# Performance work log

Measured on AMD Instinct MI355X. Metric: run time of the kernel, lower is better.

## Reference

```python
import jax, jax.numpy as jnp
import numpy as np

N_NODES = 50000
N_EDGES = 800000
IN_CH = 256
OUT_CH = 128
HID = 2 * OUT_CH  # 256
N_GRAPHS = 64


def setup_inputs() -> dict:
    key = jax.random.key(0)
    k = jax.random.split(key, 8)
    x = jax.random.normal(k[0], (N_NODES, IN_CH), dtype=jnp.float32)
    edge_index = jax.random.randint(k[1], (2, N_EDGES), 0, N_NODES, dtype=jnp.int64)
    batch = jnp.sort(jax.random.randint(k[2], (N_NODES,), 0, N_GRAPHS, dtype=jnp.int64))
    # GCNConv parameters (glorot-ish init)
    W1 = jax.random.normal(k[3], (IN_CH, HID), dtype=jnp.float32) / np.sqrt(IN_CH)
    b1 = jnp.zeros((HID,), dtype=jnp.float32)
    W2 = jax.random.normal(k[4], (HID, OUT_CH), dtype=jnp.float32) / np.sqrt(HID)
    b2 = jnp.zeros((OUT_CH,), dtype=jnp.float32)
    return {"x": x, "W1": W1, "b1": b1, "W2": W2, "b2": b2,
            "edge_index": edge_index, "batch": batch}


def _gcn_conv(x, W, b, src, dst, n):
    """PyG GCNConv: transform, then sym-normalized aggregation with self-loops."""
    h = x @ W  # [N, F_out]
    # degree over destination nodes, including the added self-loop
    deg = jnp.zeros((n,), dtype=h.dtype).at[dst].add(1.0) + 1.0
    dinv = jax.lax.rsqrt(deg)
    norm = dinv[src] * dinv[dst]            # [E]
    agg = jnp.zeros_like(h).at[dst].add(h[src] * norm[:, None])
    agg = agg + h * (1.0 / deg)[:, None]    # self-loop contribution: deg_i^{-1}
    return agg + b


def reference(x, W1, b1, W2, b2, edge_index, batch):
    src, dst = edge_index[0], edge_index[1]
    # dropout is identity in eval mode (training=False)
    h = jax.nn.elu(_gcn_conv(x, W1, b1, src, dst, N_NODES))
    h = _gcn_conv(h, W2, b2, src, dst, N_NODES)
    # global mean pool over graphs
    ones = jnp.ones((N_NODES,), dtype=h.dtype)
    counts = jax.ops.segment_sum(ones, batch, num_segments=N_GRAPHS)
    sums = jax.ops.segment_sum(h, batch, num_segments=N_GRAPHS)
    return sums / jnp.maximum(counts, 1.0)[:, None]
```

## Files before the change

### kernel.cpp

```cpp
#include <hip/hip_runtime.h>
#include <hip/hip_bf16.h>

#define N_NODES 50000
#define N_EDGES 800000
#define IN_CH 256
#define HID 256
#define OUT_CH 128
#define N_GRAPHS 64
#define SCAN_BLOCKS 196
#define M_PAD 50048
#define POOL_CHUNK 32
#define POOL_BLOCKS ((N_NODES + POOL_CHUNK - 1) / POOL_CHUNK)

typedef __bf16 bf16x8 __attribute__((ext_vector_type(8)));
typedef float f32x4 __attribute__((ext_vector_type(4)));

__device__ __forceinline__ float bf2f(unsigned short u) {
    union { unsigned int i; float f; } x; x.i = ((unsigned int)u) << 16; return x.f;
}
__device__ __forceinline__ unsigned short f2bf(float f) {
    union { float f; unsigned int i; } x; x.f = f;
    unsigned int r = x.i + 0x7FFFu + ((x.i >> 16) & 1u);
    return (unsigned short)(r >> 16);
}

__device__ __forceinline__ void load16(const void* g, void* l) {
    __builtin_amdgcn_global_load_lds(
        (const __attribute__((address_space(1))) void*)g,
        (__attribute__((address_space(3))) void*)l, 16, 0, 0);
}

__global__ __launch_bounds__(256) void count_kernel(const int* __restrict__ ei,
                                                    int* __restrict__ cnt) {
    int e = blockIdx.x * 256 + threadIdx.x;
    if (e < N_EDGES) atomicAdd(&cnt[ei[N_EDGES + e]], 1);
}

__global__ __launch_bounds__(256) void scan_a_kernel(const int* __restrict__ cnt,
                                                     int* __restrict__ rowptr,
                                                     int* __restrict__ blocksum,
                                                     float* __restrict__ dinv,
                                                     float* __restrict__ invdeg) {
    __shared__ int tmp[256];
    int t = threadIdx.x;
    int i = blockIdx.x * 256 + t;
    int v = (i < N_NODES) ? cnt[i] : 0;
    int x = v;
    tmp[t] = x;
    __syncthreads();
#pragma unroll
    for (int off = 1; off < 256; off <<= 1) {
        int y = (t >= off) ? tmp[t - off] : 0;
        __syncthreads();
        x += y;
        tmp[t] = x;
        __syncthreads();
    }
    if (i < N_NODES) {
        rowptr[i] = x - v;
        float d = (float)v + 1.0f;
        dinv[i] = rsqrtf(d);
        invdeg[i] = 1.0f / d;
    }
    if (t == 255) blocksum[blockIdx.x] = x;
}

__global__ __launch_bounds__(256) void scan_b_kernel(const int* __restrict__ blocksum,
                                                     int* __restrict__ blockoff,
                                                     int* __restrict__ rowptr) {
    __shared__ int tmp[256];
    int t = threadIdx.x;
    int v = (t < SCAN_BLOCKS) ? blocksum[t] : 0;
    int x = v;
    tmp[t] = x;
    __syncthreads();
#pragma unroll
    for (int off = 1; off < 256; off <<= 1) {
        int y = (t >= off) ? tmp[t - off] : 0;
        __syncthreads();
        x += y;
        tmp[t] = x;
        __syncthreads();
    }
    if (t < SCAN_BLOCKS) blockoff[t] = x - v;
    if (t == 255) rowptr[N_NODES] = x;
}

__global__ __launch_bounds__(256) void scan_c_kernel(int* __restrict__ rowptr,
                                                     const int* __restrict__ blockoff) {
    int i = blockIdx.x * 256 + threadIdx.x;
    if (i < N_NODES) rowptr[i] += blockoff[blockIdx.x];
}

__global__ __launch_bounds__(256) void fill_kernel(const int* __restrict__ ei,
                                                   const int* __restrict__ rowptr,
                                                   int* __restrict__ fillp,
                                                   int2* __restrict__ edge2,
                                                   const float* __restrict__ dinv) {
    int e = blockIdx.x * 256 + threadIdx.x;
    if (e >= N_EDGES) return;
    int s = ei[e];
    int d = ei[N_EDGES + e];
    int p = rowptr[d] + atomicAdd(&fillp[d], 1);
    float w = dinv[s] * dinv[d];
    edge2[p] = make_int2(s, __float_as_int(w));
}

__global__ __launch_bounds__(256) void cvt_x_kernel(const float* __restrict__ x,
                                                    unsigned short* __restrict__ xb) {
    int i = blockIdx.x * 256 + threadIdx.x;
    if (i >= M_PAD * (IN_CH / 4)) return;
    ushort4 o;
    if (i < N_NODES * (IN_CH / 4)) {
        float4 v = ((const float4*)x)[i];
        o.x = f2bf(v.x); o.y = f2bf(v.y); o.z = f2bf(v.z); o.w = f2bf(v.w);
    } else {
        o = make_ushort4(0, 0, 0, 0);
    }
    ((ushort4*)xb)[i] = o;
}

__global__ __launch_bounds__(256) void cvt_w_kernel(const float* __restrict__ W1,
                                                    const float* __restrict__ W2,
                                                    unsigned short* __restrict__ w1t,
                                                    unsigned short* __restrict__ w2t) {
    int i = blockIdx.x * 256 + threadIdx.x;
    if (i < HID * IN_CH) {
        int n = i >> 8, k = i & 255;
        w1t[i] = f2bf(W1[k * HID + n]);
    } else if (i < HID * IN_CH + OUT_CH * HID) {
        int j = i - HID * IN_CH;
        int n = j >> 8, k = j & 255;
        w2t[j] = f2bf(W2[k * OUT_CH + n]);
    }
}

__global__ __launch_bounds__(256) void gemm_mfma_kernel(
        const unsigned short* __restrict__ A,
        const unsigned short* __restrict__ Bt,
        unsigned short* __restrict__ C,
        int N) {
    const int K = 256;
    __shared__ char As[8192];
    __shared__ char Bs[8192];
    int tid = threadIdx.x;
    int bm = blockIdx.x * 128;
    int bn = blockIdx.y * 128;
    int lane = tid & 63, wave = tid >> 6;
    int lane15 = lane & 15, quad = lane >> 4;
    int wm0 = (wave >> 1) << 6;
    int wn0 = (wave & 1) << 6;

    int s1 = tid, s2 = tid + 256;
    int r1 = s1 >> 2, q1 = (s1 & 3) ^ ((r1 >> 1) & 3);
    int r2 = s2 >> 2, q2 = (s2 & 3) ^ ((r2 >> 1) & 3);
    const char* gA1 = (const char*)(A + (size_t)(bm + r1) * K) + (q1 << 4);
    const char* gA2 = (const char*)(A + (size_t)(bm + r2) * K) + (q2 << 4);
    const char* gB1 = (const char*)(Bt + (size_t)(bn + r1) * K) + (q1 << 4);
    const char* gB2 = (const char*)(Bt + (size_t)(bn + r2) * K) + (q2 << 4);
    char* lA1 = As + (wave << 10);
    char* lA2 = As + 4096 + (wave << 10);
    char* lB1 = Bs + (wave << 10);
    char* lB2 = Bs + 4096 + (wave << 10);

    int swm = (lane15 >> 1) & 3;
    f32x4 acc[4][4];
#pragma unroll
    for (int mt = 0; mt < 4; mt++)
#pragma unroll
        for (int nt = 0; nt < 4; nt++)
            acc[mt][nt] = (f32x4){0.f, 0.f, 0.f, 0.f};

    for (int k0 = 0; k0 < K; k0 += 32) {
        __syncthreads();
        load16(gA1 + (k0 << 1), lA1);
        load16(gA2 + (k0 << 1), lA2);
        load16(gB1 + (k0 << 1), lB1);
        load16(gB2 + (k0 << 1), lB2);
        __syncthreads();
        bf16x8 af[4], bfr[4];
#pragma unroll
        for (int t = 0; t < 4; t++) {
            int ra = wm0 + t * 16 + lane15;
            af[t] = *(const bf16x8*)(As + ra * 64 + ((quad ^ swm) << 4));
            int rb = wn0 + t * 16 + lane15;
            bfr[t] = *(const bf16x8*)(Bs + rb * 64 + ((quad ^ swm) << 4));
        }
#pragma unroll
        for (int mt = 0; mt < 4; mt++)
#pragma unroll
            for (int nt = 0; nt < 4; nt++)
                acc[mt][nt] = __builtin_amdgcn_mfma_f32_16x16x32_bf16(
                    af[mt], bfr[nt], acc[mt][nt], 0, 0, 0);
    }

#pragma unroll
    for (int mt = 0; mt < 4; mt++) {
        int rowb = bm + wm0 + mt * 16 + quad * 4;
#pragma unroll
        for (int nt = 0; nt < 4; nt++) {
            int col = bn + wn0 + nt * 16 + lane15;
            f32x4 a = acc[mt][nt];
            C[(size_t)(rowb + 0) * N + col] = f2bf(a[0]);
            C[(size_t)(rowb + 1) * N + col] = f2bf(a[1]);
            C[(size_t)(rowb + 2) * N + col] = f2bf(a[2]);
            C[(size_t)(rowb + 3) * N + col] = f2bf(a[3]);
        }
    }
}

__global__ __launch_bounds__(256) void agg1_kernel(const unsigned short* __restrict__ h,
                                                   const float* __restrict__ bias,
                                                   const int* __restrict__ rowptr,
                                                   const int2* __restrict__ edge2,
                                                   const float* __restrict__ invdeg,
                                                   unsigned short* __restrict__ out) {
    int node = blockIdx.x * 4 + (threadIdx.x >> 6);
    if (node >= N_NODES) return;
    int lane = threadIdx.x & 63;
    const ushort4* h4 = (const ushort4*)h;
    float id = invdeg[node];
    ushort4 sv = h4[(size_t)node * 64 + lane];
    float4 acc = make_float4(bf2f(sv.x) * id, bf2f(sv.y) * id,
                             bf2f(sv.z) * id, bf2f(sv.w) * id);
    int e0 = rowptr[node], e1 = rowptr[node + 1];
    int e = e0;
    for (; e + 1 < e1; e += 2) {
        int2 ed0 = edge2[e], ed1 = edge2[e + 1];
        float w0 = __int_as_float(ed0.y), w1 = __int_as_float(ed1.y);
        ushort4 v0 = h4[(size_t)ed0.x * 64 + lane];
        ushort4 v1 = h4[(size_t)ed1.x * 64 + lane];
        acc.x += bf2f(v0.x) * w0; acc.y += bf2f(v0.y) * w0;
        acc.z += bf2f(v0.z) * w0; acc.w += bf2f(v0.w) * w0;
        acc.x += bf2f(v1.x) * w1; acc.y += bf2f(v1.y) * w1;
        acc.z += bf2f(v1.z) * w1; acc.w += bf2f(v1.w) * w1;
    }
    if (e < e1) {
        int2 ed0 = edge2[e];
        float w0 = __int_as_float(ed0.y);
        ushort4 v0 = h4[(size_t)ed0.x * 64 + lane];
        acc.x += bf2f(v0.x) * w0; acc.y += bf2f(v0.y) * w0;
        acc.z += bf2f(v0.z) * w0; acc.w += bf2f(v0.w) * w0;
    }
    float4 bb = ((const float4*)bias)[lane];
    acc.x += bb.x; acc.y += bb.y; acc.z += bb.z; acc.w += bb.w;
    acc.x = acc.x > 0.f ? acc.x : expm1f(acc.x);
    acc.y = acc.y > 0.f ? acc.y : expm1f(acc.y);
    acc.z = acc.z > 0.f ? acc.z : expm1f(acc.z);
    acc.w = acc.w > 0.f ? acc.w : expm1f(acc.w);
    ushort4 o;
    o.x = f2bf(acc.x); o.y = f2bf(acc.y); o.z = f2bf(acc.z); o.w = f2bf(acc.w);
    ((ushort4*)out)[(size_t)node * 64 + lane] = o;
}

__global__ __launch_bounds__(256) void agg2_kernel(const unsigned short* __restrict__ h,
                                                   const float* __restrict__ bias,
                                                   const int* __restrict__ rowptr,
                                                   const int2* __restrict__ edge2,
                                                   const float* __restrict__ invdeg,
                                                   float* __restrict__ out) {
    int node = blockIdx.x * 4 + (threadIdx.x >> 6);
    if (node >= N_NODES) return;
    int lane = threadIdx.x & 63;
    const ushort2* h2 = (const ushort2*)h;
    float id = invdeg[node];
    ushort2 sv = h2[(size_t)node * 64 + lane];
    float2 acc = make_float2(bf2f(sv.x) * id, bf2f(sv.y) * id);
    int e0 = rowptr[node], e1 = rowptr[node + 1];
    int e = e0;
    for (; e + 1 < e1; e += 2) {
        int2 ed0 = edge2[e], ed1 = edge2[e + 1];
        float w0 = __int_as_float(ed0.y), w1 = __int_as_float(ed1.y);
        ushort2 v0 = h2[(size_t)ed0.x * 64 + lane];
        ushort2 v1 = h2[(size_t)ed1.x * 64 + lane];
        acc.x += bf2f(v0.x) * w0; acc.y += bf2f(v0.y) * w0;
        acc.x += bf2f(v1.x) * w1; acc.y += bf2f(v1.y) * w1;
    }
    if (e < e1) {
        int2 ed0 = edge2[e];
        float w0 = __int_as_float(ed0.y);
        ushort2 v0 = h2[(size_t)ed0.x * 64 + lane];
        acc.x += bf2f(v0.x) * w0; acc.y += bf2f(v0.y) * w0;
    }
    float2 bb = ((const float2*)bias)[lane];
    acc.x += bb.x; acc.y += bb.y;
    ((float2*)out)[(size_t)node * 64 + lane] = acc;
}

__global__ __launch_bounds__(128) void pool_kernel(const float* __restrict__ h,
                                                   const int* __restrict__ batch,
                                                   float* __restrict__ pool,
                                                   float* __restrict__ gcnt) {
    int c = threadIdx.x;
    int n0 = blockIdx.x * POOL_CHUNK;
    int n1 = n0 + POOL_CHUNK;
    if (n1 > N_NODES) n1 = N_NODES;
    if (n0 >= N_NODES) return;
    float run = 0.f, cnt = 0.f;
    int g = batch[n0];
    for (int n = n0; n < n1; n++) {
        int gn = batch[n];
        if (gn != g) {
            atomicAdd(&pool[g * OUT_CH + c], run);
            if (c == 0) atomicAdd(&gcnt[g], cnt);
            run = 0.f; cnt = 0.f; g = gn;
        }
        run += h[(size_t)n * OUT_CH + c];
        if (c == 0) cnt += 1.f;
    }
    atomicAdd(&pool[g * OUT_CH + c], run);
    if (c == 0) atomicAdd(&gcnt[g], cnt);
}

__global__ __launch_bounds__(256) void final_kernel(const float* __restrict__ pool,
                                                    const float* __restrict__ gcnt,
                                                    float* __restrict__ out) {
    int i = blockIdx.x * 256 + threadIdx.x;
    if (i < N_GRAPHS * OUT_CH)
        out[i] = pool[i] / fmaxf(gcnt[i >> 7], 1.0f);
}

extern "C" void kernel_launch(void* const* d_in, const int* in_sizes, int n_in,
                              void* d_out, int out_size, void* d_ws, size_t ws_size,
                              hipStream_t stream) {
    const float* x  = (const float*)d_in[0];
    const float* W1 = (const float*)d_in[1];
    const float* b1 = (const float*)d_in[2];
    const float* W2 = (const float*)d_in[3];
    const float* b2 = (const float*)d_in[4];
    const int*   ei = (const int*)d_in[5];
    const int*   batch = (const int*)d_in[6];
    float* out = (float*)d_out;

    unsigned short* xb  = (unsigned short*)d_ws;
    unsigned short* h1b = xb  + (size_t)M_PAD * HID;
    unsigned short* hBb = h1b + (size_t)M_PAD * HID;
    unsigned short* h2b = hBb + (size_t)M_PAD * HID;
    unsigned short* w1t = h2b + (size_t)M_PAD * OUT_CH;
    unsigned short* w2t = w1t + HID * IN_CH;
    float* hC  = (float*)xb;
    float* dinv   = (float*)(w2t + OUT_CH * HID);
    float* invdeg = dinv + N_NODES;
    int*   rowptr = (int*)(invdeg + N_NODES);
    int2*  edge2  = (int2*)(rowptr + 50016);
    int*   cnt    = (int*)(edge2 + N_EDGES);
    int*   fillp  = cnt + N_NODES;
    float* gcnt   = (float*)(fillp + N_NODES);
    float* pool   = gcnt + N_GRAPHS;
    int*   blocksum = (int*)(pool + N_GRAPHS * OUT_CH);
    int*   blockoff = blocksum + 256;

    size_t zbytes = ((size_t)N_NODES * 2 + N_GRAPHS + (size_t)N_GRAPHS * OUT_CH) * 4;
    hipMemsetAsync(cnt, 0, zbytes, stream);

    count_kernel<<<(N_EDGES + 255) / 256, 256, 0, stream>>>(ei, cnt);
    scan_a_kernel<<<SCAN_BLOCKS, 256, 0, stream>>>(cnt, rowptr, blocksum, dinv, invdeg);
    scan_b_kernel<<<1, 256, 0, stream>>>(blocksum, blockoff, rowptr);
    scan_c_kernel<<<SCAN_BLOCKS, 256, 0, stream>>>(rowptr, blockoff);
    fill_kernel<<<(N_EDGES + 255) / 256, 256, 0, stream>>>(ei, rowptr, fillp, edge2, dinv);

    cvt_x_kernel<<<(M_PAD * (IN_CH / 4) + 255) / 256, 256, 0, stream>>>(x, xb);
    cvt_w_kernel<<<(HID * IN_CH + OUT_CH * HID + 255) / 256, 256, 0, stream>>>(W1, W2, w1t, w2t);

    dim3 g1(M_PAD / 128, HID / 128);
    gemm_mfma_kernel<<<g1, 256, 0, stream>>>(xb, w1t, h1b, HID);
    agg1_kernel<<<(N_NODES + 3) / 4, 256, 0, stream>>>(h1b, b1, rowptr, edge2, invdeg, hBb);

    dim3 g2(M_PAD / 128, OUT_CH / 128);
    gemm_mfma_kernel<<<g2, 256, 0, stream>>>(hBb, w2t, h2b, OUT_CH);
    agg2_kernel<<<(N_NODES + 3) / 4, 256, 0, stream>>>(h2b, b2, rowptr, edge2, invdeg, hC);

    pool_kernel<<<POOL_BLOCKS, 128, 0, stream>>>(hC, batch, pool, gcnt);
    final_kernel<<<(N_GRAPHS * OUT_CH + 255) / 256, 256, 0, stream>>>(pool, gcnt, out);
}
```

Baseline: 356.8 us.

## Fuse fp32-to-bf16 conversion into first GEMM, unroll aggregation gathers, bf16 layer-2 output

Drops the separate x-conversion kernel. The first GEMM now loads fp32 rows of x directly, converts them to bf16 in registers and stores them into LDS, which removes a full write and re-read of the converted x buffer. The gather loops in both aggregation kernels are unrolled to 8 and 4 edges, with all loads issued before the accumulates, to keep more memory requests in flight. The layer-2 aggregation output is stored as bf16 instead of fp32, halving the traffic into pooling at some precision cost. The trade-off is that A-tile loads in the first GEMM become synchronous register loads instead of async LDS loads, and the extra unrolling raises register pressure.

```diff
diff --git a/kernel.cpp b/kernel.cpp
--- a/kernel.cpp
+++ b/kernel.cpp
@@ -14,6 +14,7 @@
 
 typedef __bf16 bf16x8 __attribute__((ext_vector_type(8)));
 typedef float f32x4 __attribute__((ext_vector_type(4)));
+typedef unsigned short u16x8 __attribute__((ext_vector_type(8)));
 
 __device__ __forceinline__ float bf2f(unsigned short u) {
     union { unsigned int i; float f; } x; x.i = ((unsigned int)u) << 16; return x.f;
@@ -104,20 +105,6 @@
     int p = rowptr[d] + atomicAdd(&fillp[d], 1);
     float w = dinv[s] * dinv[d];
     edge2[p] = make_int2(s, __float_as_int(w));
-}
-
-__global__ __launch_bounds__(256) void cvt_x_kernel(const float* __restrict__ x,
-                                                    unsigned short* __restrict__ xb) {
-    int i = blockIdx.x * 256 + threadIdx.x;
-    if (i >= M_PAD * (IN_CH / 4)) return;
-    ushort4 o;
-    if (i < N_NODES * (IN_CH / 4)) {
-        float4 v = ((const float4*)x)[i];
-        o.x = f2bf(v.x); o.y = f2bf(v.y); o.z = f2bf(v.z); o.w = f2bf(v.w);
-    } else {
-        o = make_ushort4(0, 0, 0, 0);
-    }
-    ((ushort4*)xb)[i] = o;
 }
 
 __global__ __launch_bounds__(256) void cvt_w_kernel(const float* __restrict__ W1,
@@ -208,6 +195,93 @@
         }
     }
 }
+
+__global__ __launch_bounds__(256) void gemm_mfma_x_kernel(
+        const float* __restrict__ A,
+        const unsigned short* __restrict__ Bt,
+        unsigned short* __restrict__ C,
+        int N) {
+    const int K = 256;
+    __shared__ char As[8192];
+    __shared__ char Bs[8192];
+    int tid = threadIdx.x;
+    int bm = blockIdx.x * 128;
+    int bn = blockIdx.y * 128;
+    int lane = tid & 63, wave = tid >> 6;
+    int lane15 = lane & 15, quad = lane >> 4;
+    int wm0 = (wave >> 1) << 6;
+    int wn0 = (wave & 1) << 6;
+
+    int s1 = tid, s2 = tid + 256;
+    int r1 = s1 >> 2, q1 = (s1 & 3) ^ ((r1 >> 1) & 3);
+    int r2 = s2 >> 2, q2 = (s2 & 3) ^ ((r2 >> 1) & 3);
+    const bool in1 = (bm + r1) < N_NODES;
+    const bool in2 = (bm + r2) < N_NODES;
+    const float* gA1 = A + (size_t)(bm + r1) * K + (q1 << 3);
+    const float* gA2 = A + (size_t)(bm + r2) * K + (q2 << 3);
+    const char* gB1 = (const char*)(Bt + (size_t)(bn + r1) * K) + (q1 << 4);
+    const char* gB2 = (const char*)(Bt + (size_t)(bn + r2) * K) + (q2 << 4);
+    char* lB1 = Bs + (wave << 10);
+    char* lB2 = Bs + 4096 + (wave << 10);
+
+    int swm = (lane15 >> 1) & 3;
+    f32x4 acc[4][4];
+#pragma unroll
+    for (int mt = 0; mt < 4; mt++)
+#pragma unroll
+        for (int nt = 0; nt < 4; nt++)
+            acc[mt][nt] = (f32x4){0.f, 0.f, 0.f, 0.f};
+
+    const float4 z4 = make_float4(0.f, 0.f, 0.f, 0.f);
+    for (int k0 = 0; k0 < K; k0 += 32) {
+        __syncthreads();
+        load16(gB1 + (k0 << 1), lB1);
+        load16(gB2 + (k0 << 1), lB2);
+        float4 a0 = in1 ? *(const float4*)(gA1 + k0)     : z4;
+        float4 a1 = in1 ? *(const float4*)(gA1 + k0 + 4) : z4;
+        float4 a2 = in2 ? *(const float4*)(gA2 + k0)     : z4;
+        float4 a3 = in2 ? *(const float4*)(gA2 + k0 + 4) : z4;
+        u16x8 u1 = { f2bf(a0.x), f2bf(a0.y), f2bf(a0.z), f2bf(a0.w),
+                     f2bf(a1.x), f2bf(a1.y), f2bf(a1.z), f2bf(a1.w) };
+        u16x8 u2 = { f2bf(a2.x), f2bf(a2.y), f2bf(a2.z), f2bf(a2.w),
+                     f2bf(a3.x), f2bf(a3.y), f2bf(a3.z), f2bf(a3.w) };
+        *(u16x8*)(As + s1 * 16) = u1;
+        *(u16x8*)(As + s2 * 16) = u2;
+        __syncthreads();
+        bf16x8 af[4], bfr[4];
+#pragma unroll
+        for (int t = 0; t < 4; t++) {
+            int ra = wm0 + t * 16 + lane15;
+            af[t] = *(const bf16x8*)(As + ra * 64 + ((quad ^ swm) << 4));
+            int rb = wn0 + t * 16 + lane15;
+            bfr[t] = *(const bf16x8*)(Bs + rb * 64 + ((quad ^ swm) << 4));
+        }
+#pragma unroll
+        for (int mt = 0; mt < 4; mt++)
+#pragma unroll
+            for (int nt = 0; nt < 4; nt++)
+                acc[mt][nt] = __builtin_amdgcn_mfma_f32_16x16x32_bf16(
+                    af[mt], bfr[nt], acc[mt][nt], 0, 0, 0);
+    }
+
+#pragma unroll
+    for (int mt = 0; mt < 4; mt++) {
+        int rowb = bm + wm0 + mt * 16 + quad * 4;
+#pragma unroll
+        for (int nt = 0; nt < 4; nt++) {
+            int col = bn + wn0 + nt * 16 + lane15;
+            f32x4 a = acc[mt][nt];
+            C[(size_t)(rowb + 0) * N + col] = f2bf(a[0]);
+            C[(size_t)(rowb + 1) * N + col] = f2bf(a[1]);
+            C[(size_t)(rowb + 2) * N + col] = f2bf(a[2]);
+            C[(size_t)(rowb + 3) * N + col] = f2bf(a[3]);
+        }
+    }
+}
+
+#define ACC4(V, W) \
+    acc.x += bf2f(V.x) * W; acc.y += bf2f(V.y) * W; \
+    acc.z += bf2f(V.z) * W; acc.w += bf2f(V.w) * W;
 
 __global__ __launch_bounds__(256) void agg1_kernel(const unsigned short* __restrict__ h,
                                                    const float* __restrict__ bias,
@@ -225,22 +299,37 @@
                              bf2f(sv.z) * id, bf2f(sv.w) * id);
     int e0 = rowptr[node], e1 = rowptr[node + 1];
     int e = e0;
-    for (; e + 1 < e1; e += 2) {
-        int2 ed0 = edge2[e], ed1 = edge2[e + 1];
-        float w0 = __int_as_float(ed0.y), w1 = __int_as_float(ed1.y);
-        ushort4 v0 = h4[(size_t)ed0.x * 64 + lane];
-        ushort4 v1 = h4[(size_t)ed1.x * 64 + lane];
-        acc.x += bf2f(v0.x) * w0; acc.y += bf2f(v0.y) * w0;
-        acc.z += bf2f(v0.z) * w0; acc.w += bf2f(v0.w) * w0;
-        acc.x += bf2f(v1.x) * w1; acc.y += bf2f(v1.y) * w1;
-        acc.z += bf2f(v1.z) * w1; acc.w += bf2f(v1.w) * w1;
-    }
-    if (e < e1) {
+    for (; e + 7 < e1; e += 8) {
+        int2 ed[8];
+        ushort4 v[8];
+#pragma unroll
+        for (int j = 0; j < 8; j++) ed[j] = edge2[e + j];
+#pragma unroll
+        for (int j = 0; j < 8; j++) v[j] = h4[(size_t)ed[j].x * 64 + lane];
+#pragma unroll
+        for (int j = 0; j < 8; j++) {
+            float w = __int_as_float(ed[j].y);
+            ACC4(v[j], w);
+        }
+    }
+    for (; e + 3 < e1; e += 4) {
+        int2 ed[4];
+        ushort4 v[4];
+#pragma unroll
+        for (int j = 0; j < 4; j++) ed[j] = edge2[e + j];
+#pragma unroll
+        for (int j = 0; j < 4; j++) v[j] = h4[(size_t)ed[j].x * 64 + lane];
+#pragma unroll
+        for (int j = 0; j < 4; j++) {
+            float w = __int_as_float(ed[j].y);
+            ACC4(v[j], w);
+        }
+    }
+    for (; e < e1; e++) {
         int2 ed0 = edge2[e];
         float w0 = __int_as_float(ed0.y);
         ushort4 v0 = h4[(size_t)ed0.x * 64 + lane];
-        acc.x += bf2f(v0.x) * w0; acc.y += bf2f(v0.y) * w0;
-        acc.z += bf2f(v0.z) * w0; acc.w += bf2f(v0.w) * w0;
+        ACC4(v0, w0);
     }
     float4 bb = ((const float4*)bias)[lane];
     acc.x += bb.x; acc.y += bb.y; acc.z += bb.z; acc.w += bb.w;
@@ -253,12 +342,15 @@
     ((ushort4*)out)[(size_t)node * 64 + lane] = o;
 }
 
+#define ACC2(V, W) \
+    acc.x += bf2f(V.x) * W; acc.y += bf2f(V.y) * W;
+
 __global__ __launch_bounds__(256) void agg2_kernel(const unsigned short* __restrict__ h,
                                                    const float* __restrict__ bias,
                                                    const int* __restrict__ rowptr,
                                                    const int2* __restrict__ edge2,
                                                    const float* __restrict__ invdeg,
-                                                   float* __restrict__ out) {
+                                                   unsigned short* __restrict__ out) {
     int node = blockIdx.x * 4 + (threadIdx.x >> 6);
     if (node >= N_NODES) return;
     int lane = threadIdx.x & 63;
@@ -268,26 +360,46 @@
     float2 acc = make_float2(bf2f(sv.x) * id, bf2f(sv.y) * id);
     int e0 = rowptr[node], e1 = rowptr[node + 1];
     int e = e0;
-    for (; e + 1 < e1; e += 2) {
-        int2 ed0 = edge2[e], ed1 = edge2[e + 1];
-        float w0 = __int_as_float(ed0.y), w1 = __int_as_float(ed1.y);
-        ushort2 v0 = h2[(size_t)ed0.x * 64 + lane];
-        ushort2 v1 = h2[(size_t)ed1.x * 64 + lane];
-        acc.x += bf2f(v0.x) * w0; acc.y += bf2f(v0.y) * w0;
-        acc.x += bf2f(v1.x) * w1; acc.y += bf2f(v1.y) * w1;
-    }
-    if (e < e1) {
+    for (; e + 7 < e1; e += 8) {
+        int2 ed[8];
+        ushort2 v[8];
+#pragma unroll
+        for (int j = 0; j < 8; j++) ed[j] = edge2[e + j];
+#pragma unroll
+        for (int j = 0; j < 8; j++) v[j] = h2[(size_t)ed[j].x * 64 + lane];
+#pragma unroll
+        for (int j = 0; j < 8; j++) {
+            float w = __int_as_float(ed[j].y);
+            ACC2(v[j], w);
+        }
+    }
+    for (; e + 3 < e1; e += 4) {
+        int2 ed[4];
+        ushort2 v[4];
+#pragma unroll
+        for (int j = 0; j < 4; j++) ed[j] = edge2[e + j];
+#pragma unroll
+        for (int j = 0; j < 4; j++) v[j] = h2[(size_t)ed[j].x * 64 + lane];
+#pragma unroll
+        for (int j = 0; j < 4; j++) {
+            float w = __int_as_float(ed[j].y);
+            ACC2(v[j], w);
+        }
+    }
+    for (; e < e1; e++) {
         int2 ed0 = edge2[e];
         float w0 = __int_as_float(ed0.y);
         ushort2 v0 = h2[(size_t)ed0.x * 64 + lane];
-        acc.x += bf2f(v0.x) * w0; acc.y += bf2f(v0.y) * w0;
+        ACC2(v0, w0);
     }
     float2 bb = ((const float2*)bias)[lane];
     acc.x += bb.x; acc.y += bb.y;
-    ((float2*)out)[(size_t)node * 64 + lane] = acc;
-}
-
-__global__ __launch_bounds__(128) void pool_kernel(const float* __restrict__ h,
+    ushort2 o;
+    o.x = f2bf(acc.x); o.y = f2bf(acc.y);
+    ((ushort2*)out)[(size_t)node * 64 + lane] = o;
+}
+
+__global__ __launch_bounds__(128) void pool_kernel(const unsigned short* __restrict__ h,
                                                    const int* __restrict__ batch,
                                                    float* __restrict__ pool,
                                                    float* __restrict__ gcnt) {
@@ -305,7 +417,7 @@
             if (c == 0) atomicAdd(&gcnt[g], cnt);
             run = 0.f; cnt = 0.f; g = gn;
         }
-        run += h[(size_t)n * OUT_CH + c];
+        run += bf2f(h[(size_t)n * OUT_CH + c]);
         if (c == 0) cnt += 1.f;
     }
     atomicAdd(&pool[g * OUT_CH + c], run);
@@ -332,13 +444,12 @@
     const int*   batch = (const int*)d_in[6];
     float* out = (float*)d_out;
 
-    unsigned short* xb  = (unsigned short*)d_ws;
-    unsigned short* h1b = xb  + (size_t)M_PAD * HID;
+    unsigned short* h1b = (unsigned short*)d_ws;
     unsigned short* hBb = h1b + (size_t)M_PAD * HID;
     unsigned short* h2b = hBb + (size_t)M_PAD * HID;
     unsigned short* w1t = h2b + (size_t)M_PAD * OUT_CH;
     unsigned short* w2t = w1t + HID * IN_CH;
-    float* hC  = (float*)xb;
+    unsigned short* hcb = h1b;
     float* dinv   = (float*)(w2t + OUT_CH * HID);
     float* invdeg = dinv + N_NODES;
     int*   rowptr = (int*)(invdeg + N_NODES);
@@ -359,17 +470,16 @@
     scan_c_kernel<<<SCAN_BLOCKS, 256, 0, stream>>>(rowptr, blockoff);
     fill_kernel<<<(N_EDGES + 255) / 256, 256, 0, stream>>>(ei, rowptr, fillp, edge2, dinv);
 
-    cvt_x_kernel<<<(M_PAD * (IN_CH / 4) + 255) / 256, 256, 0, stream>>>(x, xb);
     cvt_w_kernel<<<(HID * IN_CH + OUT_CH * HID + 255) / 256, 256, 0, stream>>>(W1, W2, w1t, w2t);
 
     dim3 g1(M_PAD / 128, HID / 128);
-    gemm_mfma_kernel<<<g1, 256, 0, stream>>>(xb, w1t, h1b, HID);
+    gemm_mfma_x_kernel<<<g1, 256, 0, stream>>>(x, w1t, h1b, HID);
     agg1_kernel<<<(N_NODES + 3) / 4, 256, 0, stream>>>(h1b, b1, rowptr, edge2, invdeg, hBb);
 
     dim3 g2(M_PAD / 128, OUT_CH / 128);
     gemm_mfma_kernel<<<g2, 256, 0, stream>>>(hBb, w2t, h2b, OUT_CH);
-    agg2_kernel<<<(N_NODES + 3) / 4, 256, 0, stream>>>(h2b, b2, rowptr, edge2, invdeg, hC);
-
-    pool_kernel<<<POOL_BLOCKS, 128, 0, stream>>>(hC, batch, pool, gcnt);
+    agg2_kernel<<<(N_NODES + 3) / 4, 256, 0, stream>>>(h2b, b2, rowptr, edge2, invdeg, hcb);
+
+    pool_kernel<<<POOL_BLOCKS, 128, 0, stream>>>(hcb, batch, pool, gcnt);
     final_kernel<<<(N_GRAPHS * OUT_CH + 255) / 256, 256, 0, stream>>>(pool, gcnt, out);
 }
```

After: 334.6 us. 6.2% less time.
